# Performance work log

Measured on AMD Instinct MI355X. Metric: run time of the kernel, lower is better.

The kernel has to match this reference:

```python
import jax, jax.numpy as jnp
import numpy as np

P = 512        # n_predicates
C = 65536      # n_constants
L = 1          # max_rule_length (only runnable config of original code)


def setup_inputs() -> dict:
    key = jax.random.key(0)
    k1, k2 = jax.random.split(key)
    initial_facts = jax.random.uniform(k1, (P, C), dtype=jnp.float32)
    rule_weights = jax.random.normal(k2, (P, L, P), dtype=jnp.float32)
    return {"initial_facts": initial_facts, "rule_weights": rule_weights, "n_iterations": 3}


def reference(initial_facts, rule_weights, n_iterations):
    # F.softmax(rule[step], dim=0) on the 1-D vector rule_weights[r, 0, :]
    # == softmax over the last axis of rule_weights[:, 0, :].
    # Stacking apply_rule over all rules r is exactly A @ facts.
    A = jax.nn.softmax(rule_weights[:, 0, :], axis=-1)  # [P, P]
    facts = initial_facts                                # [P, C]
    for _ in range(n_iterations):
        derived = A @ facts                              # [P, C] (rule r -> row r)
        facts = jnp.maximum(facts, derived.max(axis=0))  # broadcast [C] over [P, C]
    return facts
```

## Files before the change

### kernel.cpp

```cpp
#include <hip/hip_runtime.h>
#include <hip/hip_bf16.h>
#include <cstdint>


typedef __attribute__((ext_vector_type(8))) short bf16x8;
typedef __attribute__((ext_vector_type(8))) unsigned short u16x8;
typedef __attribute__((ext_vector_type(16))) float f32x16;
typedef unsigned short ushort_t;
typedef unsigned int uint32;

#define PDIM 512
#define CDIM 65536
#define NT   64
#define WAVES 8

__device__ __forceinline__ ushort_t f2bf(float x) {
    uint32 u = __float_as_uint(x);
    return (ushort_t)((u + 0x7fffu + ((u >> 16) & 1u)) >> 16);
}
__device__ __forceinline__ float bf2f(uint32 bits) { return __uint_as_float(bits << 16); }

__device__ __forceinline__ bf16x8 pkmax8(bf16x8 v, ushort_t mu) {
    u16x8 a = __builtin_bit_cast(u16x8, v);
    const u16x8 mb = {mu, mu, mu, mu, mu, mu, mu, mu};
    a = __builtin_elementwise_max(a, mb);
    return __builtin_bit_cast(bf16x8, a);
}

__global__ __launch_bounds__(64) void softmax_pack(const float* __restrict__ rw,
                                                   ushort_t* __restrict__ Apk) {
    const int r  = blockIdx.x;
    const int ln = threadIdx.x;
    const float* row = rw + r * PDIM;
    float4 x0 = *(const float4*)(row + ln * 8);
    float4 x1 = *(const float4*)(row + ln * 8 + 4);
    float v[8] = {x0.x, x0.y, x0.z, x0.w, x1.x, x1.y, x1.z, x1.w};

    float mx = -1e30f;
    #pragma unroll
    for (int i = 0; i < 8; ++i) mx = fmaxf(mx, v[i]);
    #pragma unroll
    for (int d = 1; d < 64; d <<= 1) mx = fmaxf(mx, __shfl_xor(mx, d, 64));
    float s = 0.f;
    #pragma unroll
    for (int i = 0; i < 8; ++i) { v[i] = __expf(v[i] - mx); s += v[i]; }
    #pragma unroll
    for (int d = 1; d < 64; d <<= 1) s += __shfl_xor(s, d, 64);
    const float inv = 1.f / s;

    ushort_t o[8];
    #pragma unroll
    for (int i = 0; i < 8; ++i) o[i] = f2bf(v[i] * inv);
    const int idx16 = ((ln >> 1) * 16 + (r >> 5)) * 64 + ((ln & 1) << 5) + (r & 31);
    *(int4*)(Apk + idx16 * 8) = *(const int4*)o;
}

__global__ __launch_bounds__(512, 4) void ilp_kernel(
        const float* __restrict__ facts,
        const ushort_t* __restrict__ Apk,
        const int* __restrict__ n_iter_p,
        float* __restrict__ out) {
    __shared__ ushort_t ft[64 * NT * 8];
    __shared__ float wred[2][WAVES][NT];
    __shared__ float mfin[NT];

    const int tid  = threadIdx.x;
    const int wave = tid >> 6;
    const int lane = tid & 63;
    const int l31  = lane & 31;
    const int half = lane >> 5;
    const int c0   = blockIdx.x * NT;

    int n_iter = *n_iter_p;
    n_iter = n_iter < 0 ? 0 : (n_iter > 8 ? 8 : n_iter);

    {
        const int c = tid & 63;
        #pragma unroll 2
        for (int s = 0; s < 8; ++s) {
            const int g = wave * 8 + s;
            ushort_t gb[8];
            #pragma unroll
            for (int i = 0; i < 8; ++i)
                gb[i] = f2bf(facts[(g * 8 + i) * CDIM + c0 + c]);
            *(int4*)(&ft[(g * 64 + c) * 8]) = *(const int4*)gb;
        }
    }

    const ushort_t* abase = Apk + (wave * 128 + half * 32 + l31) * 8;
    bf16x8 aF[2][2], bR[2][2];
    aF[0][0] = *(const bf16x8*)(abase);
    aF[0][1] = *(const bf16x8*)(abase + 512);

    __syncthreads();

    const int bbase = (half * 64 + l31) * 8;
    bR[0][0] = *(const bf16x8*)(&ft[bbase]);
    bR[0][1] = *(const bf16x8*)(&ft[bbase + 256]);

    ushort_t ml[2] = {0, 0};
    float    mf[2] = {0.f, 0.f};

    #pragma unroll 1
    for (int it = 0; it < n_iter; ++it) {
        f32x16 acc[2][2];
        #pragma unroll
        for (int rt2 = 0; rt2 < 2; ++rt2)
            #pragma unroll
            for (int ct2 = 0; ct2 < 2; ++ct2)
                #pragma unroll
                for (int e = 0; e < 16; ++e) acc[rt2][ct2][e] = 0.f;

        #pragma unroll 2
        for (int kt2 = 0; kt2 < 32; ++kt2) {
            const int cur = kt2 & 1, nxt = cur ^ 1;
            const int ktn = (kt2 + 1) & 31;
            {
                const ushort_t* ap = abase + ktn * 8192;
                aF[nxt][0] = *(const bf16x8*)(ap);
                aF[nxt][1] = *(const bf16x8*)(ap + 512);
            }
            {
                const int bo = bbase + ktn * 1024;
                bR[nxt][0] = *(const bf16x8*)(&ft[bo]);
                bR[nxt][1] = *(const bf16x8*)(&ft[bo + 256]);
            }
            __builtin_amdgcn_s_setprio(1);
            #pragma unroll
            for (int ct2 = 0; ct2 < 2; ++ct2) {
                const bf16x8 bC = pkmax8(bR[cur][ct2], ml[ct2]);
                acc[0][ct2] = __builtin_amdgcn_mfma_f32_32x32x16_bf16(
                    aF[cur][0], bC, acc[0][ct2], 0, 0, 0);
                acc[1][ct2] = __builtin_amdgcn_mfma_f32_32x32x16_bf16(
                    aF[cur][1], bC, acc[1][ct2], 0, 0, 0);
            }
            __builtin_amdgcn_s_setprio(0);
        }

        float mx[2];
        #pragma unroll
        for (int ct2 = 0; ct2 < 2; ++ct2) {
            float m0 = -1e30f;
            #pragma unroll
            for (int rt2 = 0; rt2 < 2; ++rt2)
                #pragma unroll
                for (int e = 0; e < 16; ++e) m0 = fmaxf(m0, acc[rt2][ct2][e]);
            m0 = fmaxf(m0, __shfl_xor(m0, 32, 64));
            mx[ct2] = m0;
        }
        const int buf = it & 1;
        if (half == 0) {
            #pragma unroll
            for (int ct2 = 0; ct2 < 2; ++ct2) wred[buf][wave][ct2 * 32 + l31] = mx[ct2];
        }
        __syncthreads();
        #pragma unroll
        for (int ct2 = 0; ct2 < 2; ++ct2) {
            const int c = ct2 * 32 + l31;
            float m = wred[buf][0][c];
            #pragma unroll
            for (int w = 1; w < WAVES; ++w) m = fmaxf(m, wred[buf][w][c]);
            mf[ct2] = fmaxf(mf[ct2], m);
            ml[ct2] = f2bf(mf[ct2]);
        }
    }

    if (wave == 0 && half == 0) {
        mfin[l31]      = mf[0];
        mfin[32 + l31] = mf[1];
    }
    __syncthreads();

    {
        const int c = tid & 63;
        const float m = mfin[c];
        #pragma unroll 2
        for (int s = 0; s < 8; ++s) {
            const int g = wave * 8 + s;
            ushort_t gb[8];
            *(int4*)gb = *(const int4*)(&ft[(g * 64 + c) * 8]);
            #pragma unroll
            for (int i = 0; i < 8; ++i)
                out[(g * 8 + i) * CDIM + c0 + c] = fmaxf(bf2f(gb[i]), m);
        }
    }
}

extern "C" void kernel_launch(void* const* d_in, const int* in_sizes, int n_in,
                              void* d_out, int out_size, void* d_ws, size_t ws_size,
                              hipStream_t stream) {
    const float* facts    = (const float*)d_in[0];
    const float* rw       = (const float*)d_in[1];
    const int*   n_iter_p = (const int*)d_in[2];
    float* out = (float*)d_out;

    ushort_t* Apk = (ushort_t*)d_ws;

    softmax_pack<<<PDIM, 64, 0, stream>>>(rw, Apk);
    ilp_kernel<<<CDIM / NT, 512, 0, stream>>>(facts, Apk, n_iter_p, out);
}
```

Before: 307.5 us.

## Double column tile to 128 with 16 waves, one row-tile per wave

Widens each block's column tile from 64 to 128 and uses 16 waves of 1024 threads. Each wave now owns a single 32-row tile of A and four 32-column MFMA tiles instead of two by two. The intent is to halve the per-column cost of streaming A from global memory and to halve the block count. It also reshapes the A/B prefetch pipeline: B is loaded one step ahead and A two steps ahead with a rotating buffer. In exchange, LDS use per block doubles and the 1024-thread blocks may lower occupancy or add barrier cost.

```diff
diff --git a/kernel.cpp b/kernel.cpp
--- a/kernel.cpp
+++ b/kernel.cpp
@@ -11,8 +11,8 @@
 
 #define PDIM 512
 #define CDIM 65536
-#define NT   64
-#define WAVES 8
+#define NT   128
+#define WAVES 16
 
 __device__ __forceinline__ ushort_t f2bf(float x) {
     uint32 u = __float_as_uint(x);
@@ -55,7 +55,7 @@
     *(int4*)(Apk + idx16 * 8) = *(const int4*)o;
 }
 
-__global__ __launch_bounds__(512, 4) void ilp_kernel(
+__global__ __launch_bounds__(1024, 4) void ilp_kernel(
         const float* __restrict__ facts,
         const ushort_t* __restrict__ Apk,
         const int* __restrict__ n_iter_p,
@@ -75,87 +75,84 @@
     n_iter = n_iter < 0 ? 0 : (n_iter > 8 ? 8 : n_iter);
 
     {
-        const int c = tid & 63;
+        const int c   = tid & 127;
+        const int grp = tid >> 7;
         #pragma unroll 2
         for (int s = 0; s < 8; ++s) {
-            const int g = wave * 8 + s;
+            const int g = grp * 8 + s;
             ushort_t gb[8];
             #pragma unroll
             for (int i = 0; i < 8; ++i)
                 gb[i] = f2bf(facts[(g * 8 + i) * CDIM + c0 + c]);
-            *(int4*)(&ft[(g * 64 + c) * 8]) = *(const int4*)gb;
+            *(int4*)(&ft[(g * NT + c) * 8]) = *(const int4*)gb;
         }
     }
 
-    const ushort_t* abase = Apk + (wave * 128 + half * 32 + l31) * 8;
-    bf16x8 aF[2][2], bR[2][2];
-    aF[0][0] = *(const bf16x8*)(abase);
-    aF[0][1] = *(const bf16x8*)(abase + 512);
+    const ushort_t* abase = Apk + (wave * 64 + half * 32 + l31) * 8;
+    bf16x8 aF[2], bR[4];
+    aF[0] = *(const bf16x8*)(abase);
+    aF[1] = *(const bf16x8*)(abase + 8192);
 
     __syncthreads();
 
-    const int bbase = (half * 64 + l31) * 8;
-    bR[0][0] = *(const bf16x8*)(&ft[bbase]);
-    bR[0][1] = *(const bf16x8*)(&ft[bbase + 256]);
+    const int bbase = (half * NT + l31) * 8;
+    #pragma unroll
+    for (int ct2 = 0; ct2 < 4; ++ct2)
+        bR[ct2] = *(const bf16x8*)(&ft[bbase + ct2 * 256]);
 
-    ushort_t ml[2] = {0, 0};
-    float    mf[2] = {0.f, 0.f};
+    ushort_t ml[4] = {0, 0, 0, 0};
+    float    mf[4] = {0.f, 0.f, 0.f, 0.f};
 
     #pragma unroll 1
     for (int it = 0; it < n_iter; ++it) {
-        f32x16 acc[2][2];
+        f32x16 acc[4];
         #pragma unroll
-        for (int rt2 = 0; rt2 < 2; ++rt2)
+        for (int ct2 = 0; ct2 < 4; ++ct2)
             #pragma unroll
-            for (int ct2 = 0; ct2 < 2; ++ct2)
-                #pragma unroll
-                for (int e = 0; e < 16; ++e) acc[rt2][ct2][e] = 0.f;
+            for (int e = 0; e < 16; ++e) acc[ct2][e] = 0.f;
 
         #pragma unroll 2
         for (int kt2 = 0; kt2 < 32; ++kt2) {
-            const int cur = kt2 & 1, nxt = cur ^ 1;
-            const int ktn = (kt2 + 1) & 31;
+            const int cur = kt2 & 1;
+
+            bf16x8 bC[4];
+            #pragma unroll
+            for (int ct2 = 0; ct2 < 4; ++ct2) bC[ct2] = pkmax8(bR[ct2], ml[ct2]);
+
             {
-                const ushort_t* ap = abase + ktn * 8192;
-                aF[nxt][0] = *(const bf16x8*)(ap);
-                aF[nxt][1] = *(const bf16x8*)(ap + 512);
+                const int bo = bbase + ((kt2 + 1) & 31) * 2048;
+                #pragma unroll
+                for (int ct2 = 0; ct2 < 4; ++ct2)
+                    bR[ct2] = *(const bf16x8*)(&ft[bo + ct2 * 256]);
             }
-            {
-                const int bo = bbase + ktn * 1024;
-                bR[nxt][0] = *(const bf16x8*)(&ft[bo]);
-                bR[nxt][1] = *(const bf16x8*)(&ft[bo + 256]);
-            }
+
             __builtin_amdgcn_s_setprio(1);
             #pragma unroll
-            for (int ct2 = 0; ct2 < 2; ++ct2) {
-                const bf16x8 bC = pkmax8(bR[cur][ct2], ml[ct2]);
-                acc[0][ct2] = __builtin_amdgcn_mfma_f32_32x32x16_bf16(
-                    aF[cur][0], bC, acc[0][ct2], 0, 0, 0);
-                acc[1][ct2] = __builtin_amdgcn_mfma_f32_32x32x16_bf16(
-                    aF[cur][1], bC, acc[1][ct2], 0, 0, 0);
-            }
+            for (int ct2 = 0; ct2 < 4; ++ct2)
+                acc[ct2] = __builtin_amdgcn_mfma_f32_32x32x16_bf16(
+                    aF[cur], bC[ct2], acc[ct2], 0, 0, 0);
             __builtin_amdgcn_s_setprio(0);
+
+            aF[cur] = *(const bf16x8*)(abase + ((kt2 + 2) & 31) * 8192);
         }
 
-        float mx[2];
+        float mx[4];
         #pragma unroll
-        for (int ct2 = 0; ct2 < 2; ++ct2) {
+        for (int ct2 = 0; ct2 < 4; ++ct2) {
             float m0 = -1e30f;
             #pragma unroll
-            for (int rt2 = 0; rt2 < 2; ++rt2)
-                #pragma unroll
-                for (int e = 0; e < 16; ++e) m0 = fmaxf(m0, acc[rt2][ct2][e]);
+            for (int e = 0; e < 16; ++e) m0 = fmaxf(m0, acc[ct2][e]);
             m0 = fmaxf(m0, __shfl_xor(m0, 32, 64));
             mx[ct2] = m0;
         }
         const int buf = it & 1;
         if (half == 0) {
             #pragma unroll
-            for (int ct2 = 0; ct2 < 2; ++ct2) wred[buf][wave][ct2 * 32 + l31] = mx[ct2];
+            for (int ct2 = 0; ct2 < 4; ++ct2) wred[buf][wave][ct2 * 32 + l31] = mx[ct2];
         }
         __syncthreads();
         #pragma unroll
-        for (int ct2 = 0; ct2 < 2; ++ct2) {
+        for (int ct2 = 0; ct2 < 4; ++ct2) {
             const int c = ct2 * 32 + l31;
             float m = wred[buf][0][c];
             #pragma unroll
@@ -166,19 +163,20 @@
     }
 
     if (wave == 0 && half == 0) {
-        mfin[l31]      = mf[0];
-        mfin[32 + l31] = mf[1];
+        #pragma unroll
+        for (int ct2 = 0; ct2 < 4; ++ct2) mfin[ct2 * 32 + l31] = mf[ct2];
     }
     __syncthreads();
 
     {
-        const int c = tid & 63;
+        const int c   = tid & 127;
+        const int grp = tid >> 7;
         const float m = mfin[c];
         #pragma unroll 2
         for (int s = 0; s < 8; ++s) {
-            const int g = wave * 8 + s;
+            const int g = grp * 8 + s;
             ushort_t gb[8];
-            *(int4*)gb = *(const int4*)(&ft[(g * 64 + c) * 8]);
+            *(int4*)gb = *(const int4*)(&ft[(g * NT + c) * 8]);
             #pragma unroll
             for (int i = 0; i < 8; ++i)
                 out[(g * 8 + i) * CDIM + c0 + c] = fmaxf(bf2f(gb[i]), m);
@@ -197,5 +195,5 @@
     ushort_t* Apk = (ushort_t*)d_ws;
 
     softmax_pack<<<PDIM, 64, 0, stream>>>(rw, Apk);
-    ilp_kernel<<<CDIM / NT, 512, 0, stream>>>(facts, Apk, n_iter_p, out);
+    ilp_kernel<<<CDIM / NT, 1024, 0, stream>>>(facts, Apk, n_iter_p, out);
 }
```

Measured after the change: 332.1 us. +8.0%, slower.
